# Kernel tuning notes

Measured on AMD Instinct MI355X. Metric: run time of the kernel, lower is better.

## Reference

```python
import jax, jax.numpy as jnp
import numpy as np


def _nn_idx(query, ref):
    """Index of nearest ref point for each query point.
    query: [B,N,3], ref: [B,M,3] -> idx [B,N] (int32).
    Squared distance via ||q||^2 - 2 q.r + ||r||^2 (matches cdist+top1).
    """
    d2 = (jnp.sum(query * query, axis=-1, keepdims=True)
          - 2.0 * jnp.einsum('bnd,bmd->bnm', query, ref)
          + jnp.sum(ref * ref, axis=-1)[:, None, :])
    return jnp.argmin(d2, axis=-1)


def setup_inputs() -> dict:
    key = jax.random.key(0)
    k1, k2, k3 = jax.random.split(key, 3)
    B, N, M = 1, 16384, 16384  # batch hard-coded to 1 in original loops
    pred = jax.random.normal(k1, (B, N, 3), dtype=jnp.float32)
    gt = jax.random.normal(k2, (B, M, 3), dtype=jnp.float32)
    weight = jax.random.uniform(k3, (1,), dtype=jnp.float32)
    return {"pred": pred, "gt": gt, "weight": weight}


def reference(pred, gt, weight):
    # get_mse_loss2: weighted bidirectional nearest-neighbor MSE.
    w = weight[0]
    # B2A: align each pred point to its nearest gt point
    idx = _nn_idx(pred, gt)                                   # [B,N]
    align_gt = jnp.take_along_axis(gt, idx[..., None], axis=1)  # [B,N,3]
    B2A = jnp.mean((pred - align_gt) ** 2)
    # A2B: align each gt point to its nearest pred point
    idx2 = _nn_idx(gt, pred)                                  # [B,M]
    align_out = jnp.take_along_axis(pred, idx2[..., None], axis=1)  # [B,M,3]
    A2B = jnp.mean((align_out - gt) ** 2)
    return B2A * w + A2B * (1.0 - w)
```

## Files before the change

### kernel.cpp

```cpp
#include <hip/hip_runtime.h>


#define NPTS   16384
#define QBLK   256
#define QCH    (NPTS / QBLK)
#define SSPLIT 8
#define RBLK   (NPTS / SSPLIT)
#define NB1    (2 * QCH * SSPLIT)

typedef __attribute__((ext_vector_type(8)))  __bf16 bf16x8;
typedef __attribute__((ext_vector_type(16))) float  floatx16;

union frag16 { __bf16 v[16]; uint4 q[2]; };

__global__ __launch_bounds__(256) void prep_kernel(
    const float* __restrict__ pred, const float* __restrict__ gt,
    uint4* __restrict__ aform, uint4* __restrict__ bform,
    float* __restrict__ out)
{
    const int i = blockIdx.x * 256 + threadIdx.x;
    if (i == 0) out[0] = 0.0f;
    const int role = (i < NPTS) ? 0 : 1;
    const int p = i - role * NPTS;
    const float* __restrict__ src = role ? gt : pred;

    const float x = src[p * 3 + 0], y = src[p * 3 + 1], z = src[p * 3 + 2];
    const float nn = x * x + y * y + z * z;
    const __bf16 xh = (__bf16)x, yh = (__bf16)y, zh = (__bf16)z;
    const __bf16 xl = (__bf16)(x - (float)xh);
    const __bf16 yl = (__bf16)(y - (float)yh);
    const __bf16 zl = (__bf16)(z - (float)zh);
    const __bf16 nh = (__bf16)nn;
    const __bf16 nl = (__bf16)(nn - (float)nh);
    const __bf16 one = (__bf16)1.0f;

    frag16 A;
    A.v[0]  = (__bf16)(-2.0f * (float)xh); A.v[1]  = A.v[0];
    A.v[2]  = (__bf16)(-2.0f * (float)xl); A.v[3]  = A.v[2];
    A.v[4]  = (__bf16)(-2.0f * (float)yh); A.v[5]  = A.v[4];
    A.v[6]  = (__bf16)(-2.0f * (float)yl); A.v[7]  = A.v[6];
    A.v[8]  = (__bf16)(-2.0f * (float)zh); A.v[9]  = A.v[8];
    A.v[10] = (__bf16)(-2.0f * (float)zl); A.v[11] = A.v[10];
    A.v[12] = nh;  A.v[13] = nl;  A.v[14] = one;  A.v[15] = one;

    frag16 B;
    B.v[0] = xh;  B.v[1]  = xl;  B.v[2]  = xh;  B.v[3]  = xl;
    B.v[4] = yh;  B.v[5]  = yl;  B.v[6]  = yh;  B.v[7]  = yl;
    B.v[8] = zh;  B.v[9]  = zl;  B.v[10] = zh;  B.v[11] = zl;
    B.v[12] = one; B.v[13] = one; B.v[14] = nh;  B.v[15] = nl;

    uint4* da = aform + (size_t)role * (NPTS * 2)
              + ((p >> 5) * 64 + (p & 31));
    da[0]  = A.q[0];
    da[32] = A.q[1];
    uint4* db = bform + (size_t)role * (NPTS * 2) + p * 2;
    db[0] = B.q[0];
    db[1] = B.q[1];
}

#define MFMA_MIN_BLOCK(BQ, M)                                               \
    asm volatile(                                                           \
        "v_mfma_f32_32x32x16_bf16 v[32:47], %[A0], %[B], %[Z]\n\t"          \
        "v_mfma_f32_32x32x16_bf16 v[48:63], %[A1], %[B], %[Z]\n\t"          \
        "s_nop 7\n\ts_nop 7\n\ts_nop 7\n\ts_nop 7\n\t"                      \
        "v_min3_f32 %[M0],  %[M0],  v32, v48\n\t"                           \
        "v_min3_f32 %[M1],  %[M1],  v33, v49\n\t"                           \
        "v_min3_f32 %[M2],  %[M2],  v34, v50\n\t"                           \
        "v_min3_f32 %[M3],  %[M3],  v35, v51\n\t"                           \
        "v_min3_f32 %[M4],  %[M4],  v36, v52\n\t"                           \
        "v_min3_f32 %[M5],  %[M5],  v37, v53\n\t"                           \
        "v_min3_f32 %[M6],  %[M6],  v38, v54\n\t"                           \
        "v_min3_f32 %[M7],  %[M7],  v39, v55\n\t"                           \
        "v_min3_f32 %[M8],  %[M8],  v40, v56\n\t"                           \
        "v_min3_f32 %[M9],  %[M9],  v41, v57\n\t"                           \
        "v_min3_f32 %[M10], %[M10], v42, v58\n\t"                           \
        "v_min3_f32 %[M11], %[M11], v43, v59\n\t"                           \
        "v_min3_f32 %[M12], %[M12], v44, v60\n\t"                           \
        "v_min3_f32 %[M13], %[M13], v45, v61\n\t"                           \
        "v_min3_f32 %[M14], %[M14], v46, v62\n\t"                           \
        "v_min3_f32 %[M15], %[M15], v47, v63"                               \
        : [M0] "+v"(M[0]),  [M1] "+v"(M[1]),  [M2] "+v"(M[2]),              \
          [M3] "+v"(M[3]),  [M4] "+v"(M[4]),  [M5] "+v"(M[5]),              \
          [M6] "+v"(M[6]),  [M7] "+v"(M[7]),  [M8] "+v"(M[8]),              \
          [M9] "+v"(M[9]),  [M10] "+v"(M[10]), [M11] "+v"(M[11]),           \
          [M12] "+v"(M[12]), [M13] "+v"(M[13]), [M14] "+v"(M[14]),          \
          [M15] "+v"(M[15])                                                 \
        : [A0] "v"(a0), [A1] "v"(a1), [B] "v"(BQ), [Z] "v"(zero)            \
        : "v32", "v33", "v34", "v35", "v36", "v37", "v38", "v39",           \
          "v40", "v41", "v42", "v43", "v44", "v45", "v46", "v47",           \
          "v48", "v49", "v50", "v51", "v52", "v53", "v54", "v55",           \
          "v56", "v57", "v58", "v59", "v60", "v61", "v62", "v63")

__global__ __launch_bounds__(256) void nn_part_kernel(
    const uint4* __restrict__ aform, const uint4* __restrict__ bform,
    float* __restrict__ partial)
{
    const int bx   = blockIdx.x;
    const int dir  = bx >> 9;
    const int qc   = (bx & 511) >> 3;
    const int s    = bx & 7;
    const int tid  = threadIdx.x;
    const int lane = tid & 63;
    const int wave = tid >> 6;
    const int lid  = lane & 31;
    const int half = lane >> 5;

    const uint4* __restrict__ Aref = aform + (size_t)(dir ? 0 : 1) * (NPTS * 2);
    const uint4* __restrict__ Bqry = bform + (size_t)(dir ? 1 : 0) * (NPTS * 2);

    const int qbase = qc * QBLK + wave * 64;
    const bf16x8 bq0 = __builtin_bit_cast(bf16x8, Bqry[(qbase + lid) * 2 + half]);
    const bf16x8 bq1 = __builtin_bit_cast(bf16x8, Bqry[(qbase + 32 + lid) * 2 + half]);

    floatx16 zero;
#pragma unroll
    for (int k = 0; k < 16; ++k) zero[k] = 0.0f;

    float ma[16], mb[16];
#pragma unroll
    for (int k = 0; k < 16; ++k) { ma[k] = 3.4e38f; mb[k] = 3.4e38f; }

    const uint4* gp = Aref + (size_t)s * (RBLK * 2) + half * 32 + lid;
#pragma unroll 2
    for (int t = 0; t < RBLK / 32; t += 2) {
        const bf16x8 a0 = __builtin_bit_cast(bf16x8, gp[t * 64]);
        const bf16x8 a1 = __builtin_bit_cast(bf16x8, gp[t * 64 + 64]);
        MFMA_MIN_BLOCK(bq0, ma);
        MFMA_MIN_BLOCK(bq1, mb);
    }

    float* pout = partial + ((size_t)((dir * QCH + qc) * SSPLIT + s)) * QBLK
                + wave * 64;
    {
        float a = fminf(fminf(ma[0], ma[1]), fminf(ma[2], ma[3]));
        float b = fminf(fminf(ma[4], ma[5]), fminf(ma[6], ma[7]));
        float c = fminf(fminf(ma[8], ma[9]), fminf(ma[10], ma[11]));
        float d = fminf(fminf(ma[12], ma[13]), fminf(ma[14], ma[15]));
        float v = fminf(fminf(a, b), fminf(c, d));
        v = fminf(v, __shfl_xor(v, 32));
        if (half == 0) pout[lid] = v;
    }
    {
        float a = fminf(fminf(mb[0], mb[1]), fminf(mb[2], mb[3]));
        float b = fminf(fminf(mb[4], mb[5]), fminf(mb[6], mb[7]));
        float c = fminf(fminf(mb[8], mb[9]), fminf(mb[10], mb[11]));
        float d = fminf(fminf(mb[12], mb[13]), fminf(mb[14], mb[15]));
        float v = fminf(fminf(a, b), fminf(c, d));
        v = fminf(v, __shfl_xor(v, 32));
        if (half == 0) pout[32 + lid] = v;
    }
}

__global__ __launch_bounds__(256) void nn_combine_kernel(
    const float* __restrict__ partial, const float* __restrict__ weight,
    float* __restrict__ out)
{
    const int b   = blockIdx.x;
    const int dir = b >> 6;
    const int qc  = b & 63;
    const int t   = threadIdx.x;

    const float* p = partial + ((size_t)((dir * QCH + qc) * SSPLIT)) * QBLK;
    float v = p[t];
#pragma unroll
    for (int s = 1; s < SSPLIT; ++s)
        v = fminf(v, p[s * QBLK + t]);

    for (int off = 32; off; off >>= 1) v += __shfl_down(v, off);
    __shared__ float ws[4];
    if ((t & 63) == 0) ws[t >> 6] = v;
    __syncthreads();
    if (t == 0) {
        const float sum = ws[0] + ws[1] + ws[2] + ws[3];
        const float wgt = weight[0];
        const float scale = (dir ? (1.0f - wgt) : wgt) / (3.0f * (float)NPTS);
        atomicAdd(out, sum * scale);
    }
}

extern "C" void kernel_launch(void* const* d_in, const int* in_sizes, int n_in,
                              void* d_out, int out_size, void* d_ws, size_t ws_size,
                              hipStream_t stream) {
    const float* pred   = (const float*)d_in[0];
    const float* gt     = (const float*)d_in[1];
    const float* weight = (const float*)d_in[2];

    float* partial = (float*)d_ws;
    uint4* aform = (uint4*)((char*)d_ws + (size_t)2 * QCH * SSPLIT * QBLK * 4);
    uint4* bform = aform + (size_t)2 * NPTS * 2;

    prep_kernel<<<2 * NPTS / 256, 256, 0, stream>>>(pred, gt, aform, bform,
                                                    (float*)d_out);
    nn_part_kernel<<<NB1, 256, 0, stream>>>(aform, bform, partial);
    nn_combine_kernel<<<2 * QCH, 256, 0, stream>>>(partial, weight, (float*)d_out);
}
```

Baseline: 81.17 us.

## Software-pipeline MFMA and min3 across query halves, double the reference split

Replaces the MFMA-then-nop-then-min block with two interleaved asm blocks. Each block issues MFMAs into one register set while running min3 on the results the other set produced in the previous step, which removes the s_nop stalls from the inner loop. It also uses the inline zero constant for the accumulator, drops the zero vector register, and adds an epilogue to drain the last pending results. SSPLIT goes from 8 to 16 for more blocks. The cost is more hard-wired VGPRs (v32-v95) and a reliance on MFMA latency being covered by the interleaved work, with no explicit hazard nops inside the loop.

```diff
diff --git a/kernel.cpp b/kernel.cpp
--- a/kernel.cpp
+++ b/kernel.cpp
@@ -4,12 +4,11 @@
 #define NPTS   16384
 #define QBLK   256
 #define QCH    (NPTS / QBLK)
-#define SSPLIT 8
+#define SSPLIT 16
 #define RBLK   (NPTS / SSPLIT)
 #define NB1    (2 * QCH * SSPLIT)
 
 typedef __attribute__((ext_vector_type(8)))  __bf16 bf16x8;
-typedef __attribute__((ext_vector_type(16))) float  floatx16;
 
 union frag16 { __bf16 v[16]; uint4 q[2]; };
 
@@ -58,11 +57,46 @@
     db[1] = B.q[1];
 }
 
-#define MFMA_MIN_BLOCK(BQ, M)                                               \
+#define MFMA_A_MIN_B(A0, A1, BQ0, MB)                                       \
     asm volatile(                                                           \
-        "v_mfma_f32_32x32x16_bf16 v[32:47], %[A0], %[B], %[Z]\n\t"          \
-        "v_mfma_f32_32x32x16_bf16 v[48:63], %[A1], %[B], %[Z]\n\t"          \
-        "s_nop 7\n\ts_nop 7\n\ts_nop 7\n\ts_nop 7\n\t"                      \
+        "v_mfma_f32_32x32x16_bf16 v[32:47], %[a0], %[b], 0\n\t"             \
+        "v_mfma_f32_32x32x16_bf16 v[48:63], %[a1], %[b], 0\n\t"             \
+        "v_min3_f32 %[M0],  %[M0],  v64, v80\n\t"                           \
+        "v_min3_f32 %[M1],  %[M1],  v65, v81\n\t"                           \
+        "v_min3_f32 %[M2],  %[M2],  v66, v82\n\t"                           \
+        "v_min3_f32 %[M3],  %[M3],  v67, v83\n\t"                           \
+        "v_min3_f32 %[M4],  %[M4],  v68, v84\n\t"                           \
+        "v_min3_f32 %[M5],  %[M5],  v69, v85\n\t"                           \
+        "v_min3_f32 %[M6],  %[M6],  v70, v86\n\t"                           \
+        "v_min3_f32 %[M7],  %[M7],  v71, v87\n\t"                           \
+        "v_min3_f32 %[M8],  %[M8],  v72, v88\n\t"                           \
+        "v_min3_f32 %[M9],  %[M9],  v73, v89\n\t"                           \
+        "v_min3_f32 %[M10], %[M10], v74, v90\n\t"                           \
+        "v_min3_f32 %[M11], %[M11], v75, v91\n\t"                           \
+        "v_min3_f32 %[M12], %[M12], v76, v92\n\t"                           \
+        "v_min3_f32 %[M13], %[M13], v77, v93\n\t"                           \
+        "v_min3_f32 %[M14], %[M14], v78, v94\n\t"                           \
+        "v_min3_f32 %[M15], %[M15], v79, v95"                               \
+        : [M0] "+v"(MB[0]),  [M1] "+v"(MB[1]),  [M2] "+v"(MB[2]),           \
+          [M3] "+v"(MB[3]),  [M4] "+v"(MB[4]),  [M5] "+v"(MB[5]),           \
+          [M6] "+v"(MB[6]),  [M7] "+v"(MB[7]),  [M8] "+v"(MB[8]),           \
+          [M9] "+v"(MB[9]),  [M10] "+v"(MB[10]), [M11] "+v"(MB[11]),        \
+          [M12] "+v"(MB[12]), [M13] "+v"(MB[13]), [M14] "+v"(MB[14]),       \
+          [M15] "+v"(MB[15])                                                \
+        : [a0] "v"(A0), [a1] "v"(A1), [b] "v"(BQ0)                          \
+        : "v32", "v33", "v34", "v35", "v36", "v37", "v38", "v39",           \
+          "v40", "v41", "v42", "v43", "v44", "v45", "v46", "v47",           \
+          "v48", "v49", "v50", "v51", "v52", "v53", "v54", "v55",           \
+          "v56", "v57", "v58", "v59", "v60", "v61", "v62", "v63",           \
+          "v64", "v65", "v66", "v67", "v68", "v69", "v70", "v71",           \
+          "v72", "v73", "v74", "v75", "v76", "v77", "v78", "v79",           \
+          "v80", "v81", "v82", "v83", "v84", "v85", "v86", "v87",           \
+          "v88", "v89", "v90", "v91", "v92", "v93", "v94", "v95")
+
+#define MFMA_B_MIN_A(A0, A1, BQ1, MA)                                       \
+    asm volatile(                                                           \
+        "v_mfma_f32_32x32x16_bf16 v[64:79], %[a0], %[b], 0\n\t"             \
+        "v_mfma_f32_32x32x16_bf16 v[80:95], %[a1], %[b], 0\n\t"             \
         "v_min3_f32 %[M0],  %[M0],  v32, v48\n\t"                           \
         "v_min3_f32 %[M1],  %[M1],  v33, v49\n\t"                           \
         "v_min3_f32 %[M2],  %[M2],  v34, v50\n\t"                           \
@@ -79,26 +113,30 @@
         "v_min3_f32 %[M13], %[M13], v45, v61\n\t"                           \
         "v_min3_f32 %[M14], %[M14], v46, v62\n\t"                           \
         "v_min3_f32 %[M15], %[M15], v47, v63"                               \
-        : [M0] "+v"(M[0]),  [M1] "+v"(M[1]),  [M2] "+v"(M[2]),              \
-          [M3] "+v"(M[3]),  [M4] "+v"(M[4]),  [M5] "+v"(M[5]),              \
-          [M6] "+v"(M[6]),  [M7] "+v"(M[7]),  [M8] "+v"(M[8]),              \
-          [M9] "+v"(M[9]),  [M10] "+v"(M[10]), [M11] "+v"(M[11]),           \
-          [M12] "+v"(M[12]), [M13] "+v"(M[13]), [M14] "+v"(M[14]),          \
-          [M15] "+v"(M[15])                                                 \
-        : [A0] "v"(a0), [A1] "v"(a1), [B] "v"(BQ), [Z] "v"(zero)            \
+        : [M0] "+v"(MA[0]),  [M1] "+v"(MA[1]),  [M2] "+v"(MA[2]),           \
+          [M3] "+v"(MA[3]),  [M4] "+v"(MA[4]),  [M5] "+v"(MA[5]),           \
+          [M6] "+v"(MA[6]),  [M7] "+v"(MA[7]),  [M8] "+v"(MA[8]),           \
+          [M9] "+v"(MA[9]),  [M10] "+v"(MA[10]), [M11] "+v"(MA[11]),        \
+          [M12] "+v"(MA[12]), [M13] "+v"(MA[13]), [M14] "+v"(MA[14]),       \
+          [M15] "+v"(MA[15])                                                \
+        : [a0] "v"(A0), [a1] "v"(A1), [b] "v"(BQ1)                          \
         : "v32", "v33", "v34", "v35", "v36", "v37", "v38", "v39",           \
           "v40", "v41", "v42", "v43", "v44", "v45", "v46", "v47",           \
           "v48", "v49", "v50", "v51", "v52", "v53", "v54", "v55",           \
-          "v56", "v57", "v58", "v59", "v60", "v61", "v62", "v63")
+          "v56", "v57", "v58", "v59", "v60", "v61", "v62", "v63",           \
+          "v64", "v65", "v66", "v67", "v68", "v69", "v70", "v71",           \
+          "v72", "v73", "v74", "v75", "v76", "v77", "v78", "v79",           \
+          "v80", "v81", "v82", "v83", "v84", "v85", "v86", "v87",           \
+          "v88", "v89", "v90", "v91", "v92", "v93", "v94", "v95")
 
 __global__ __launch_bounds__(256) void nn_part_kernel(
     const uint4* __restrict__ aform, const uint4* __restrict__ bform,
     float* __restrict__ partial)
 {
     const int bx   = blockIdx.x;
-    const int dir  = bx >> 9;
-    const int qc   = (bx & 511) >> 3;
-    const int s    = bx & 7;
+    const int dir  = bx >> 10;
+    const int qc   = (bx >> 4) & 63;
+    const int s    = bx & 15;
     const int tid  = threadIdx.x;
     const int lane = tid & 63;
     const int wave = tid >> 6;
@@ -112,22 +150,70 @@
     const bf16x8 bq0 = __builtin_bit_cast(bf16x8, Bqry[(qbase + lid) * 2 + half]);
     const bf16x8 bq1 = __builtin_bit_cast(bf16x8, Bqry[(qbase + 32 + lid) * 2 + half]);
 
-    floatx16 zero;
-#pragma unroll
-    for (int k = 0; k < 16; ++k) zero[k] = 0.0f;
-
     float ma[16], mb[16];
 #pragma unroll
     for (int k = 0; k < 16; ++k) { ma[k] = 3.4e38f; mb[k] = 3.4e38f; }
+
+    asm volatile(
+        "v_mov_b32 v64, 0x7F7FFFFF\n\tv_mov_b32 v65, 0x7F7FFFFF\n\t"
+        "v_mov_b32 v66, 0x7F7FFFFF\n\tv_mov_b32 v67, 0x7F7FFFFF\n\t"
+        "v_mov_b32 v68, 0x7F7FFFFF\n\tv_mov_b32 v69, 0x7F7FFFFF\n\t"
+        "v_mov_b32 v70, 0x7F7FFFFF\n\tv_mov_b32 v71, 0x7F7FFFFF\n\t"
+        "v_mov_b32 v72, 0x7F7FFFFF\n\tv_mov_b32 v73, 0x7F7FFFFF\n\t"
+        "v_mov_b32 v74, 0x7F7FFFFF\n\tv_mov_b32 v75, 0x7F7FFFFF\n\t"
+        "v_mov_b32 v76, 0x7F7FFFFF\n\tv_mov_b32 v77, 0x7F7FFFFF\n\t"
+        "v_mov_b32 v78, 0x7F7FFFFF\n\tv_mov_b32 v79, 0x7F7FFFFF\n\t"
+        "v_mov_b32 v80, 0x7F7FFFFF\n\tv_mov_b32 v81, 0x7F7FFFFF\n\t"
+        "v_mov_b32 v82, 0x7F7FFFFF\n\tv_mov_b32 v83, 0x7F7FFFFF\n\t"
+        "v_mov_b32 v84, 0x7F7FFFFF\n\tv_mov_b32 v85, 0x7F7FFFFF\n\t"
+        "v_mov_b32 v86, 0x7F7FFFFF\n\tv_mov_b32 v87, 0x7F7FFFFF\n\t"
+        "v_mov_b32 v88, 0x7F7FFFFF\n\tv_mov_b32 v89, 0x7F7FFFFF\n\t"
+        "v_mov_b32 v90, 0x7F7FFFFF\n\tv_mov_b32 v91, 0x7F7FFFFF\n\t"
+        "v_mov_b32 v92, 0x7F7FFFFF\n\tv_mov_b32 v93, 0x7F7FFFFF\n\t"
+        "v_mov_b32 v94, 0x7F7FFFFF\n\tv_mov_b32 v95, 0x7F7FFFFF"
+        ::: "v64", "v65", "v66", "v67", "v68", "v69", "v70", "v71",
+            "v72", "v73", "v74", "v75", "v76", "v77", "v78", "v79",
+            "v80", "v81", "v82", "v83", "v84", "v85", "v86", "v87",
+            "v88", "v89", "v90", "v91", "v92", "v93", "v94", "v95");
 
     const uint4* gp = Aref + (size_t)s * (RBLK * 2) + half * 32 + lid;
 #pragma unroll 2
     for (int t = 0; t < RBLK / 32; t += 2) {
         const bf16x8 a0 = __builtin_bit_cast(bf16x8, gp[t * 64]);
         const bf16x8 a1 = __builtin_bit_cast(bf16x8, gp[t * 64 + 64]);
-        MFMA_MIN_BLOCK(bq0, ma);
-        MFMA_MIN_BLOCK(bq1, mb);
-    }
+        MFMA_A_MIN_B(a0, a1, bq0, mb);
+        MFMA_B_MIN_A(a0, a1, bq1, ma);
+    }
+
+    asm volatile(
+        "s_nop 7\n\ts_nop 7\n\ts_nop 7\n\ts_nop 7\n\t"
+        "v_min3_f32 %[M0],  %[M0],  v64, v80\n\t"
+        "v_min3_f32 %[M1],  %[M1],  v65, v81\n\t"
+        "v_min3_f32 %[M2],  %[M2],  v66, v82\n\t"
+        "v_min3_f32 %[M3],  %[M3],  v67, v83\n\t"
+        "v_min3_f32 %[M4],  %[M4],  v68, v84\n\t"
+        "v_min3_f32 %[M5],  %[M5],  v69, v85\n\t"
+        "v_min3_f32 %[M6],  %[M6],  v70, v86\n\t"
+        "v_min3_f32 %[M7],  %[M7],  v71, v87\n\t"
+        "v_min3_f32 %[M8],  %[M8],  v72, v88\n\t"
+        "v_min3_f32 %[M9],  %[M9],  v73, v89\n\t"
+        "v_min3_f32 %[M10], %[M10], v74, v90\n\t"
+        "v_min3_f32 %[M11], %[M11], v75, v91\n\t"
+        "v_min3_f32 %[M12], %[M12], v76, v92\n\t"
+        "v_min3_f32 %[M13], %[M13], v77, v93\n\t"
+        "v_min3_f32 %[M14], %[M14], v78, v94\n\t"
+        "v_min3_f32 %[M15], %[M15], v79, v95"
+        : [M0] "+v"(mb[0]),  [M1] "+v"(mb[1]),  [M2] "+v"(mb[2]),
+          [M3] "+v"(mb[3]),  [M4] "+v"(mb[4]),  [M5] "+v"(mb[5]),
+          [M6] "+v"(mb[6]),  [M7] "+v"(mb[7]),  [M8] "+v"(mb[8]),
+          [M9] "+v"(mb[9]),  [M10] "+v"(mb[10]), [M11] "+v"(mb[11]),
+          [M12] "+v"(mb[12]), [M13] "+v"(mb[13]), [M14] "+v"(mb[14]),
+          [M15] "+v"(mb[15])
+        :
+        : "v64", "v65", "v66", "v67", "v68", "v69", "v70", "v71",
+          "v72", "v73", "v74", "v75", "v76", "v77", "v78", "v79",
+          "v80", "v81", "v82", "v83", "v84", "v85", "v86", "v87",
+          "v88", "v89", "v90", "v91", "v92", "v93", "v94", "v95");
 
     float* pout = partial + ((size_t)((dir * QCH + qc) * SSPLIT + s)) * QBLK
                 + wave * 64;
@@ -164,7 +250,7 @@
     float v = p[t];
 #pragma unroll
     for (int s = 1; s < SSPLIT; ++s)
-        v = fminf(v, p[s * QBLK + t]);
+        v = fminf(v, p[(size_t)s * QBLK + t]);
 
     for (int off = 32; off; off >>= 1) v += __shfl_down(v, off);
     __shared__ float ws[4];
```

Result: no change. 80.76 us (-0.5%).
